# Kernel tuning notes

Hardware: AMD Instinct MI355X
Metric: run time of the kernel (lower is better)

## Reference

```python
import jax, jax.numpy as jnp
import numpy as np

B, D = 4096, 1024
N_CLASSES = 100
INF = jnp.float32(3.4e38)


def setup_inputs() -> dict:
    key = jax.random.key(0)
    k1, k2 = jax.random.split(key)
    x = jax.random.normal(k1, (B, 1, D), dtype=jnp.float32)
    labels = jax.random.randint(k2, (B,), 0, N_CLASSES)
    return {"x": x, "labels": labels}


def _awareness_scan(xs, labels_f, R_init):
    # xs: [B, D] float32, labels_f: [B] float32
    b, d = xs.shape
    slots = jnp.arange(b)

    def step(state, inp):
        refs, ref_labels, n_refs, count, min_d, max_d, R = state
        xi, li = inp
        mask = slots < n_refs  # active reference slots
        # distances from candidate to current reference set (torch.cdist, p=2)
        d_all = jnp.sqrt(jnp.sum((refs - xi[None, :]) ** 2, axis=-1))  # [B]
        d_all = jax.lax.stop_gradient(d_all)
        d_act = jnp.where(mask, d_all, INF)
        min_act = jnp.min(d_act)
        is_first = count == 1
        # new reference iff ALL active distances exceed R (i.e. min > R)
        insert = is_first | (min_act > R)
        refs2 = jnp.where(insert, refs.at[n_refs].set(xi), refs)
        ref_labels2 = jnp.where(insert, ref_labels.at[n_refs].set(li), ref_labels)
        n_refs2 = n_refs + insert.astype(n_refs.dtype)
        # dynamic ray update (skipped on the very first sample, as in torch)
        max_act = jnp.max(jnp.where(mask, d_all, -INF))
        min_d2 = jnp.where(is_first, min_d, jnp.minimum(min_d, min_act))
        max_d2 = jnp.where(is_first, max_d, jnp.maximum(max_d, max_act))
        R2 = jnp.where(is_first, R, (min_d2 + max_d2) / 3)
        # prediction: nearest reference AFTER potential insertion
        mask2 = slots < n_refs2
        d2 = jnp.sqrt(jnp.sum((refs2 - xi[None, :]) ** 2, axis=-1))
        d2 = jax.lax.stop_gradient(d2)
        idx = jnp.argmin(jnp.where(mask2, d2, INF))
        pred = ref_labels2[idx]
        new_state = (refs2, ref_labels2, n_refs2, count + 1, min_d2, max_d2, R2)
        return new_state, pred

    init = (
        jnp.zeros((b, d), jnp.float32),   # reference instances buffer
        jnp.zeros((b,), jnp.float32),     # reference labels buffer
        jnp.int32(0),                     # n_refs
        jnp.int32(1),                     # count (starts at 1, as in torch)
        INF,                              # min_dist
        jnp.float32(0.0),                 # max_dist
        jnp.float32(R_init),              # R
    )
    _, preds = jax.lax.scan(step, init, (xs, labels_f))
    return preds  # [B] float32


def reference(x, labels):
    # x: [B, 1, D]; labels: [B] int. update_ref_insts=True, set_labels=labels.
    xs = x.reshape(x.shape[0], x.shape[2])
    labels_f = labels.astype(jnp.float32)
    return _awareness_scan(xs, labels_f, 1.0)
```

## Files before the change

### kernel.cpp

```cpp
#include <hip/hip_runtime.h>
#include <stdint.h>

#define B_N   4096
#define D_DIM 1024
#define INF_F 3.4e38f

typedef __bf16 bf16x8 __attribute__((ext_vector_type(8)));
typedef float  floatx4 __attribute__((ext_vector_type(4)));

#define XBF_OFF 131072

__device__ inline unsigned short f2bf_rne(float f) {
    unsigned u = __float_as_uint(f);
    unsigned r = (u + 0x7FFFu + ((u >> 16) & 1u)) >> 16;
    return (unsigned short)r;
}

__global__ __launch_bounds__(256)
void k_prep(const float* __restrict__ x, unsigned short* __restrict__ xbf,
            float* __restrict__ norms,
            unsigned long long* __restrict__ minpack,
            unsigned int* __restrict__ maxbits) {
    const int row = blockIdx.x;
    const int t   = threadIdx.x;
    float4 v = ((const float4*)x)[row * 256 + t];
    ushort4 o;
    o.x = f2bf_rne(v.x); o.y = f2bf_rne(v.y);
    o.z = f2bf_rne(v.z); o.w = f2bf_rne(v.w);
    ((ushort4*)xbf)[row * 256 + t] = o;
    float s = v.x * v.x + v.y * v.y + v.z * v.z + v.w * v.w;
    #pragma unroll
    for (int off = 32; off; off >>= 1) s += __shfl_down(s, off);
    __shared__ float ws4[4];
    if ((t & 63) == 0) ws4[t >> 6] = s;
    __syncthreads();
    if (t == 0) {
        norms[row]   = ws4[0] + ws4[1] + ws4[2] + ws4[3];
        minpack[row] = 0xFFFFFFFFFFFFFFFFull;
        maxbits[row] = 0u;
    }
}

#define GLDS(g, l)                                                              \
    __builtin_amdgcn_global_load_lds(                                           \
        (__attribute__((address_space(1))) void*)(void*)(g),                    \
        (__attribute__((address_space(3))) void*)(void*)(l), 16, 0, 0)

__global__ __launch_bounds__(256, 3)
void k_pass1_mfma(const unsigned short* __restrict__ xbf,
                  const float* __restrict__ norms,
                  unsigned long long* __restrict__ minpack,
                  unsigned int* __restrict__ maxbits) {
    int bid = blockIdx.x;
    int ti  = (int)((sqrtf(8.f * bid + 1.f) - 1.f) * 0.5f);
    while ((ti + 1) * (ti + 2) / 2 <= bid) ti++;
    while (ti * (ti + 1) / 2 > bid) ti--;
    int tj  = bid - ti * (ti + 1) / 2;

    __shared__ unsigned short As[8192];
    __shared__ unsigned short Bs[8192];
    __shared__ unsigned long long redMin[128][2];
    __shared__ float redMax[128][2];

    const int t    = threadIdx.x;
    const int w    = t >> 6, lane = t & 63;
    const int wm   = w >> 1, wn = w & 1;
    const int q4   = lane >> 4, c15 = lane & 15, l7 = lane & 7;
    const int lr   = lane >> 3;
    const int kg   = (lane & 7) ^ lr;
    const int i0   = ti * 128, j0 = tj * 128;

    const unsigned short* gA[4]; const unsigned short* gB[4];
    unsigned short* lA[4]; unsigned short* lB[4];
    #pragma unroll
    for (int q = 0; q < 4; q++) {
        int e   = w * 4 + q;
        int row = e * 8 + lr;
        gA[q] = xbf + (size_t)(i0 + row) * D_DIM + kg * 8;
        gB[q] = xbf + (size_t)(j0 + row) * D_DIM + kg * 8;
        lA[q] = As + e * 512;
        lB[q] = Bs + e * 512;
    }

    int aoff[4][2], boff[4][2];
    #pragma unroll
    for (int st = 0; st < 4; st++) {
        #pragma unroll
        for (int kk = 0; kk < 2; kk++) {
            int g = ((kk * 4 + q4) ^ l7) << 4;
            aoff[st][kk] = (wm * 64 + st * 16 + c15) * 128 + g;
            boff[st][kk] = (wn * 64 + st * 16 + c15) * 128 + g;
        }
    }

    floatx4 acc[4][4];
    #pragma unroll
    for (int m = 0; m < 4; m++)
        #pragma unroll
        for (int n = 0; n < 4; n++)
            acc[m][n] = (floatx4){0.f, 0.f, 0.f, 0.f};

    for (int it = 0; it < 16; it++) {
        __syncthreads();
        #pragma unroll
        for (int q = 0; q < 4; q++) {
            GLDS(gA[q], lA[q]);
            GLDS(gB[q], lB[q]);
            gA[q] += 64; gB[q] += 64;
        }
        __syncthreads();
        #pragma unroll
        for (int kk = 0; kk < 2; kk++) {
            bf16x8 af[4], bfr[4];
            #pragma unroll
            for (int st = 0; st < 4; st++) {
                af[st]  = *(const bf16x8*)((const char*)As + aoff[st][kk]);
                bfr[st] = *(const bf16x8*)((const char*)Bs + boff[st][kk]);
            }
            #pragma unroll
            for (int m = 0; m < 4; m++)
                #pragma unroll
                for (int n = 0; n < 4; n++)
                    acc[m][n] = __builtin_amdgcn_mfma_f32_16x16x32_bf16(
                        af[m], bfr[n], acc[m][n], 0, 0, 0);
        }
    }

    float nj[4];
    #pragma unroll
    for (int st = 0; st < 4; st++) nj[st] = norms[j0 + wn * 64 + st * 16 + c15];

    #pragma unroll
    for (int st_m = 0; st_m < 4; st_m++) {
        #pragma unroll
        for (int r = 0; r < 4; r++) {
            int i_loc = wm * 64 + st_m * 16 + q4 * 4 + r;
            int gi    = i0 + i_loc;
            float ni  = norms[gi];
            unsigned long long mp = 0xFFFFFFFFFFFFFFFFull;
            float mx = -INF_F;
            #pragma unroll
            for (int st_n = 0; st_n < 4; st_n++) {
                int gj = j0 + wn * 64 + st_n * 16 + c15;
                if (gj < gi) {
                    float dot = acc[st_m][st_n][r];
                    float d   = sqrtf(fmaxf(ni + nj[st_n] - 2.f * dot, 0.f));
                    unsigned long long p =
                        ((unsigned long long)__float_as_uint(d) << 32) | (unsigned)gj;
                    if (p < mp) mp = p;
                    mx = fmaxf(mx, d);
                }
            }
            #pragma unroll
            for (int off = 1; off < 16; off <<= 1) {
                unsigned long long op = __shfl_xor(mp, off, 64);
                if (op < mp) mp = op;
                float om = __shfl_xor(mx, off, 64);
                mx = fmaxf(mx, om);
            }
            if (c15 == 0) { redMin[i_loc][wn] = mp; redMax[i_loc][wn] = mx; }
        }
    }
    __syncthreads();
    if (t < 128) {
        unsigned long long mp = redMin[t][0];
        if (redMin[t][1] < mp) mp = redMin[t][1];
        float mx = fmaxf(redMax[t][0], redMax[t][1]);
        if (mp != 0xFFFFFFFFFFFFFFFFull) {
            atomicMin(&minpack[i0 + t], mp);
            atomicMax(&maxbits[i0 + t], __float_as_uint(mx));
        }
    }
}

__global__ __launch_bounds__(1024)
void k_tail(const unsigned long long* __restrict__ minpack,
            const unsigned int* __restrict__ maxbits,
            const float* __restrict__ x, const float* __restrict__ norms,
            const int* __restrict__ labels, int* __restrict__ ref_idx,
            float* __restrict__ out) {
    const int t = threadIdx.x;
    float m[4], M[4];
    #pragma unroll
    for (int q = 0; q < 4; q++) {
        int i = t * 4 + q;
        unsigned long long p = minpack[i];
        float dmin = (p == 0xFFFFFFFFFFFFFFFFull)
                       ? INF_F : __uint_as_float((unsigned)(p >> 32));
        m[q] = (i == 0) ? INF_F : dmin;
        M[q] = (i == 0) ? -INF_F : __uint_as_float(maxbits[i]);
    }
    float pmin[4], pmax[4];
    pmin[0] = m[0]; pmax[0] = M[0];
    #pragma unroll
    for (int q = 1; q < 4; q++) {
        pmin[q] = fminf(pmin[q - 1], m[q]);
        pmax[q] = fmaxf(pmax[q - 1], M[q]);
    }
    __shared__ float smin[1024], smax[1024];
    smin[t] = pmin[3]; smax[t] = pmax[3];
    __syncthreads();
    for (int off = 1; off < 1024; off <<= 1) {
        float a = (t >= off) ? smin[t - off] : INF_F;
        float b = (t >= off) ? smax[t - off] : -INF_F;
        __syncthreads();
        smin[t] = fminf(smin[t], a);
        smax[t] = fmaxf(smax[t], b);
        __syncthreads();
    }
    float exMin = (t > 0) ? smin[t - 1] : INF_F;
    float exMax = (t > 0) ? smax[t - 1] : -INF_F;

    int viol = B_N;
    #pragma unroll
    for (int q = 0; q < 4; q++) {
        int i = t * 4 + q;
        if (i >= 1) {
            float pm = (q == 0) ? exMin : fminf(exMin, pmin[q - 1]);
            float pM = (q == 0) ? exMax : fmaxf(exMax, pmax[q - 1]);
            float R  = (i == 1) ? 1.0f : (pm + pM) / 3.0f;
            if (!(m[q] > R) && i < viol) viol = i;
        }
    }
    __shared__ int sv[1024];
    sv[t] = viol;
    __syncthreads();
    for (int off = 512; off; off >>= 1) {
        if (t < off) sv[t] = min(sv[t], sv[t + off]);
        __syncthreads();
    }
    const int s_star = sv[0];

    for (int i = t; i < s_star; i += 1024) out[i] = (float)labels[i];

    __shared__ float s_state[3];
    __shared__ int s_n;
    if (s_star < B_N && t == (s_star >> 2)) {
        int q = s_star & 3;
        float pm = (q == 0) ? exMin : fminf(exMin, pmin[q - 1]);
        float pM = (q == 0) ? exMax : fmaxf(exMax, pmax[q - 1]);
        float md = fminf(pm, m[q]);
        float Md = fmaxf(pM, M[q]);
        s_state[0] = md; s_state[1] = Md; s_state[2] = (md + Md) / 3.0f;
        s_n = s_star;
        unsigned long long p = minpack[s_star];
        int j = (int)(unsigned)(p & 0xFFFFFFFFu);
        out[s_star] = (float)labels[j];
    }
    if (s_star >= B_N) return;

    for (int s = t; s < s_star; s += 1024) ref_idx[s] = s;
    __syncthreads();

    __shared__ unsigned long long redp[1024];
    __shared__ float redm[1024];
    for (int i = s_star + 1; i < B_N; i++) {
        int n = s_n;
        const float* xi = x + (size_t)i * D_DIM;
        float ni = norms[i];
        unsigned long long mp = 0xFFFFFFFFFFFFFFFFull;
        float mx = -INF_F;
        for (int slot = t; slot < n; slot += 1024) {
            int j = ref_idx[slot];
            const float* xj = x + (size_t)j * D_DIM;
            float dot = 0.f;
            for (int k = 0; k < D_DIM; k++) dot = fmaf(xi[k], xj[k], dot);
            float d = sqrtf(fmaxf(ni + norms[j] - 2.f * dot, 0.f));
            unsigned long long p =
                ((unsigned long long)__float_as_uint(d) << 32) | (unsigned)slot;
            if (p < mp) mp = p;
            mx = fmaxf(mx, d);
        }
        redp[t] = mp; redm[t] = mx;
        __syncthreads();
        for (int off = 512; off; off >>= 1) {
            if (t < off) {
                if (redp[t + off] < redp[t]) redp[t] = redp[t + off];
                redm[t] = fmaxf(redm[t], redm[t + off]);
            }
            __syncthreads();
        }
        if (t == 0) {
            unsigned long long p = redp[0];
            float min_act = __uint_as_float((unsigned)(p >> 32));
            int minslot   = (int)(unsigned)(p & 0xFFFFFFFFu);
            float max_act = redm[0];
            bool insert = (min_act > s_state[2]);
            int pred;
            if (insert) {
                ref_idx[n] = i;
                s_n = n + 1;
                pred = (min_act <= 0.0f) ? labels[ref_idx[minslot]] : labels[i];
            } else {
                pred = labels[ref_idx[minslot]];
            }
            float md = fminf(s_state[0], min_act);
            float Md = fmaxf(s_state[1], max_act);
            s_state[0] = md; s_state[1] = Md; s_state[2] = (md + Md) / 3.0f;
            out[i] = (float)pred;
        }
        __syncthreads();
    }
}

extern "C" void kernel_launch(void* const* d_in, const int* in_sizes, int n_in,
                              void* d_out, int out_size, void* d_ws, size_t ws_size,
                              hipStream_t stream) {
    const float* x      = (const float*)d_in[0];
    const int*   labels = (const int*)d_in[1];
    float*       out    = (float*)d_out;
    char* ws = (char*)d_ws;
    unsigned long long* minpack = (unsigned long long*)ws;
    unsigned int*       maxbits = (unsigned int*)(ws + 32768);
    float*              norms   = (float*)(ws + 49152);
    int*                ref_idx = (int*)(ws + 65600);
    unsigned short*     xbf     = (unsigned short*)(ws + XBF_OFF);

    k_prep<<<B_N, 256, 0, stream>>>(x, xbf, norms, minpack, maxbits);
    const int ntiles = B_N / 128;
    const int nblocks = ntiles * (ntiles + 1) / 2;
    k_pass1_mfma<<<nblocks, 256, 0, stream>>>(xbf, norms, minpack, maxbits);
    k_tail<<<1, 1024, 0, stream>>>(minpack, maxbits, x, norms, labels, ref_idx, out);
}
```

Before: 104.3 us.

## Double-buffer LDS tiles in pairwise-distance MFMA GEMM with a smaller K step

Splits the shared-memory A/B tiles into two buffers of K=32 and prefetches the next K-slice with global_load_lds while MFMAs run on the current one. This halves the syncthreads per K-step and replaces the XOR swizzle with a new rotation-based layout. The aim is to hide global-to-LDS latency in the Gram-matrix pass. The trade-off is twice as many iterations with less MFMA work each, so the synchronization overhead per unit of compute may rise.

Result: slower. 111.4 us (+6.9%).

```diff
diff --git a/kernel.cpp b/kernel.cpp
--- a/kernel.cpp
+++ b/kernel.cpp
@@ -57,40 +57,41 @@
     while (ti * (ti + 1) / 2 > bid) ti--;
     int tj  = bid - ti * (ti + 1) / 2;
 
-    __shared__ unsigned short As[8192];
-    __shared__ unsigned short Bs[8192];
+    __shared__ unsigned short As[2][4096];
+    __shared__ unsigned short Bs[2][4096];
     __shared__ unsigned long long redMin[128][2];
     __shared__ float redMax[128][2];
 
     const int t    = threadIdx.x;
     const int w    = t >> 6, lane = t & 63;
     const int wm   = w >> 1, wn = w & 1;
-    const int q4   = lane >> 4, c15 = lane & 15, l7 = lane & 7;
-    const int lr   = lane >> 3;
-    const int kg   = (lane & 7) ^ lr;
+    const int q4   = lane >> 4, c15 = lane & 15;
     const int i0   = ti * 128, j0 = tj * 128;
 
-    const unsigned short* gA[4]; const unsigned short* gB[4];
-    unsigned short* lA[4]; unsigned short* lB[4];
-    #pragma unroll
-    for (int q = 0; q < 4; q++) {
-        int e   = w * 4 + q;
-        int row = e * 8 + lr;
-        gA[q] = xbf + (size_t)(i0 + row) * D_DIM + kg * 8;
-        gB[q] = xbf + (size_t)(j0 + row) * D_DIM + kg * 8;
-        lA[q] = As + e * 512;
-        lB[q] = Bs + e * 512;
-    }
-
-    int aoff[4][2], boff[4][2];
+    const int sr = lane >> 2;
+    const int sc = ((lane & 3) + 4 - (lane >> 4)) & 3;
+
+    const unsigned short* gA[2]; const unsigned short* gB[2];
+    unsigned short* lA[2][2]; unsigned short* lB[2][2];
+    #pragma unroll
+    for (int q = 0; q < 2; q++) {
+        int e   = w * 2 + q;
+        int row = e * 16 + sr;
+        gA[q] = xbf + (size_t)(i0 + row) * D_DIM + sc * 8;
+        gB[q] = xbf + (size_t)(j0 + row) * D_DIM + sc * 8;
+        #pragma unroll
+        for (int b = 0; b < 2; b++) {
+            lA[b][q] = &As[b][e * 512];
+            lB[b][q] = &Bs[b][e * 512];
+        }
+    }
+
+    int aoff[4], boff[4];
     #pragma unroll
     for (int st = 0; st < 4; st++) {
-        #pragma unroll
-        for (int kk = 0; kk < 2; kk++) {
-            int g = ((kk * 4 + q4) ^ l7) << 4;
-            aoff[st][kk] = (wm * 64 + st * 16 + c15) * 128 + g;
-            boff[st][kk] = (wn * 64 + st * 16 + c15) * 128 + g;
-        }
+        int sw = ((q4 + (c15 >> 2)) & 3) << 4;
+        aoff[st] = (wm * 4 + st) * 1024 + c15 * 64 + sw;
+        boff[st] = (wn * 4 + st) * 1024 + c15 * 64 + sw;
     }
 
     floatx4 acc[4][4];
@@ -100,30 +101,34 @@
         for (int n = 0; n < 4; n++)
             acc[m][n] = (floatx4){0.f, 0.f, 0.f, 0.f};
 
-    for (int it = 0; it < 16; it++) {
-        __syncthreads();
-        #pragma unroll
-        for (int q = 0; q < 4; q++) {
-            GLDS(gA[q], lA[q]);
-            GLDS(gB[q], lB[q]);
-            gA[q] += 64; gB[q] += 64;
-        }
-        __syncthreads();
-        #pragma unroll
-        for (int kk = 0; kk < 2; kk++) {
-            bf16x8 af[4], bfr[4];
+    #pragma unroll
+    for (int q = 0; q < 2; q++) { GLDS(gA[q], lA[0][q]); GLDS(gB[q], lB[0][q]); }
+
+    for (int it = 0; it < 32; it++) {
+        __syncthreads();
+        if (it < 31) {
+            const int nb = (it + 1) & 1;
             #pragma unroll
-            for (int st = 0; st < 4; st++) {
-                af[st]  = *(const bf16x8*)((const char*)As + aoff[st][kk]);
-                bfr[st] = *(const bf16x8*)((const char*)Bs + boff[st][kk]);
-            }
+            for (int q = 0; q < 2; q++) {
+                gA[q] += 32; gB[q] += 32;
+                GLDS(gA[q], lA[nb][q]);
+                GLDS(gB[q], lB[nb][q]);
+            }
+        }
+        const unsigned short* Ac = As[it & 1];
+        const unsigned short* Bc = Bs[it & 1];
+        bf16x8 af[4], bfr[4];
+        #pragma unroll
+        for (int st = 0; st < 4; st++) {
+            af[st]  = *(const bf16x8*)((const char*)Ac + aoff[st]);
+            bfr[st] = *(const bf16x8*)((const char*)Bc + boff[st]);
+        }
+        #pragma unroll
+        for (int m = 0; m < 4; m++)
             #pragma unroll
-            for (int m = 0; m < 4; m++)
-                #pragma unroll
-                for (int n = 0; n < 4; n++)
-                    acc[m][n] = __builtin_amdgcn_mfma_f32_16x16x32_bf16(
-                        af[m], bfr[n], acc[m][n], 0, 0, 0);
-        }
+            for (int n = 0; n < 4; n++)
+                acc[m][n] = __builtin_amdgcn_mfma_f32_16x16x32_bf16(
+                    af[m], bfr[n], acc[m][n], 0, 0, 0);
     }
 
     float nj[4];
@@ -317,7 +322,7 @@
     unsigned short*     xbf     = (unsigned short*)(ws + XBF_OFF);
 
     k_prep<<<B_N, 256, 0, stream>>>(x, xbf, norms, minpack, maxbits);
-    const int ntiles = B_N / 128;
+    const int ntiles  = B_N / 128;
     const int nblocks = ntiles * (ntiles + 1) / 2;
     k_pass1_mfma<<<nblocks, 256, 0, stream>>>(xbf, norms, minpack, maxbits);
     k_tail<<<1, 1024, 0, stream>>>(minpack, maxbits, x, norms, labels, ref_idx, out);
```
